# Optimization experiments

Measured on AMD Instinct MI355X. Metric: run time of the kernel, lower is better.

Reference implementation:

```python
import jax, jax.numpy as jnp
import numpy as np

B, P = 16, 1024
D_TIME, NUM_MODS = 8, 22
DIM_S = NUM_MODS + D_TIME + 1  # 31
PHI_W, N_HEADS, DP = 32, 4, 32
PSI_W, PSI_L, RHO_W = 64, 64, 64
SQRT_DP = float(np.sqrt(DP))


def setup_inputs() -> dict:
    key = jax.random.key(0)
    ks = jax.random.split(key, 16)
    rn = lambda k, shape: jax.random.normal(k, shape, jnp.float32) * 0.05
    return dict(
        times=jax.random.uniform(ks[0], (B, P), jnp.float32) * 48.0,
        values=jax.random.normal(ks[1], (B, P), jnp.float32),
        measurements=jax.random.randint(ks[2], (B, P), 0, NUM_MODS + 1),
        non_pad_mask=jnp.ones((B, P, 1), jnp.float32),
        W_psi1=rn(ks[3], (DIM_S, PSI_W)), b_psi1=jnp.zeros((PSI_W,), jnp.float32),
        W_psi2=rn(ks[4], (PSI_W, PSI_L)), b_psi2=jnp.zeros((PSI_L,), jnp.float32),
        W_key=rn(ks[5], (DIM_S + PSI_L, N_HEADS * DP)), b_key=jnp.zeros((N_HEADS * DP,), jnp.float32),
        query=rn(ks[6], (N_HEADS, DP)),
        W_phi1=rn(ks[7], (DIM_S, PHI_W)), b_phi1=jnp.zeros((PHI_W,), jnp.float32),
        W_phi2=rn(ks[8], (PHI_W, PHI_W)), b_phi2=jnp.zeros((PHI_W,), jnp.float32),
        W_rho1=rn(ks[9], (N_HEADS * PHI_W, RHO_W)), b_rho1=jnp.zeros((RHO_W,), jnp.float32),
        W_rho2=rn(ks[10], (RHO_W, RHO_W)), b_rho2=jnp.zeros((RHO_W,), jnp.float32),
    )


def _temporal_enc(times):
    i = np.arange(D_TIME)
    pos_vec = jnp.asarray(10000.0 ** (2.0 * (i // 2) / D_TIME), jnp.float32)
    ang = times[:, :, None] / pos_vec  # [B,P,d_time]
    return jnp.where(jnp.asarray(i % 2 == 0), jnp.sin(ang), jnp.cos(ang))


def reference(times, values, measurements, non_pad_mask,
              W_psi1, b_psi1, W_psi2, b_psi2, W_key, b_key, query,
              W_phi1, b_phi1, W_phi2, b_phi2, W_rho1, b_rho1, W_rho2, b_rho2):
    m = non_pad_mask  # [B,P,1]
    te = _temporal_enc(times)
    oh = jax.nn.one_hot(measurements, NUM_MODS + 1, dtype=jnp.float32)[:, :, 1:]
    x = jnp.concatenate([te, values[:, :, None], oh], axis=-1)  # [B,P,dim_s]

    # CumulativeSetAttentionLayer: psi MLP -> cumulative mean -> keys . query
    psi = jax.nn.relu(jax.nn.relu(x @ W_psi1 + b_psi1) @ W_psi2 + b_psi2)  # [B,P,psi_l]
    cum = jnp.cumsum(psi * m, axis=1) / jnp.cumsum(m, axis=1)
    keys = (jnp.concatenate([x, cum], axis=-1) @ W_key + b_key).reshape(B, P, N_HEADS, DP)
    pre = jnp.einsum('bpmd,md->bpm', keys, query) / SQRT_DP  # [B,P,m]

    # phi MLP
    phi = jax.nn.relu(jax.nn.relu(x @ W_phi1 + b_phi1) @ W_phi2 + b_phi2) * m  # [B,P,phi_w]

    # cumulative softmax weighting (online path)
    cmax = jax.lax.cummax(pre, axis=1)  # [B,P,m], running max for stability
    D = jnp.exp(pre[:, None, :, :] - cmax[:, :, None, :])  # [B,P,Q,m]
    causal = jnp.arange(P)[:, None] >= jnp.arange(P)[None, :]  # keep Q <= P
    D = D * causal[None, :, :, None]
    E = D.sum(axis=2)  # [B,P,m]
    agg = jnp.einsum('bpqm,bqd->bpmd', D, phi) / E[:, :, :, None]
    agg = (agg * m[:, :, :, None]).reshape(B, P, N_HEADS * PHI_W)

    # rho MLP (return_sequences)
    out = jax.nn.relu(jax.nn.relu(agg @ W_rho1 + b_rho1) @ W_rho2 + b_rho2) * m
    return out
```

## Files before the change

### kernel.cpp

```cpp
#include <hip/hip_runtime.h>
#include <hip/hip_bf16.h>

#define B_ 16
#define P_ 1024
#define T_ (B_*P_)
#define CH_ 32
#define CL_ (P_/CH_)

constexpr int OFF_A     = 16;
constexpr int OFF_WPSI1 = 400;
constexpr int OFF_BPSI1 = OFF_WPSI1 + 1984;
constexpr int OFF_WPSI2 = OFF_BPSI1 + 64;
constexpr int OFF_BPSI2 = OFF_WPSI2 + 4096;
constexpr int OFF_WKEY  = OFF_BPSI2 + 64;
constexpr int OFF_BKEY  = OFF_WKEY  + 12160;
constexpr int OFF_QRY   = OFF_BKEY  + 128;
constexpr int OFF_WPHI1 = OFF_QRY   + 128;
constexpr int OFF_BPHI1 = OFF_WPHI1 + 992;
constexpr int OFF_WPHI2 = OFF_BPHI1 + 32;
constexpr int OFF_BPHI2 = OFF_WPHI2 + 1024;
constexpr int OFF_WRHO1 = OFF_BPHI2 + 32;
constexpr int OFF_BRHO1 = OFF_WRHO1 + 8192;
constexpr int OFF_WRHO2 = OFF_BRHO1 + 64;
constexpr int OFF_BRHO2 = OFF_WRHO2 + 4096;
constexpr int OFF_PHI   = OFF_BRHO2 + 64;
constexpr int OFF_Z     = OFF_PHI   + T_*32;
constexpr int OFF_PREX  = OFF_Z     + T_*4;
constexpr int OFF_PRE   = OFF_PREX  + T_*4;
constexpr int OFF_AGG   = OFF_PRE   + T_*4;
constexpr int OFF_CME   = OFF_AGG   + T_*128;
constexpr int OFF_CS    = OFF_CME   + 4096;

static __device__ __forceinline__ bool detect_f32(const void* mask_raw) {
  return ((*(const unsigned*)mask_raw) & 0xFFFFu) == 0u;
}
static __device__ __forceinline__ float ld_any(const void* src, int i, bool isf32) {
  if (isf32) return ((const float*)src)[i];
  return __bfloat162float(((const __hip_bfloat16*)src)[i]);
}

__global__ __launch_bounds__(256) void s01_prep(
    float* __restrict__ ws, const void* mask,
    const void* Wpsi1, const void* bpsi1, const void* Wpsi2, const void* bpsi2,
    const void* Wkey,  const void* bkey,  const void* query,
    const void* Wphi1, const void* bphi1, const void* Wphi2, const void* bphi2,
    const void* Wrho1, const void* brho1, const void* Wrho2, const void* brho2) {
  const bool isf32 = detect_f32(mask);
  if (blockIdx.x < 2) {
    const int gid = blockIdx.x * 256 + threadIdx.x;
    if (gid >= 384) return;
    const float inv_s = 0.17677669529663687f;
    const int h = gid & 3;
    const int j = gid >> 2;
    float s = 0.f;
    if (j < 95) {
      for (int d = 0; d < 32; ++d)
        s += ld_any(Wkey, j * 128 + h * 32 + d, isf32) * ld_any(query, h * 32 + d, isf32);
    } else {
      for (int d = 0; d < 32; ++d)
        s += ld_any(bkey, h * 32 + d, isf32) * ld_any(query, h * 32 + d, isf32);
    }
    ws[OFF_A + gid] = s * inv_s;
    return;
  }
  const int g  = (blockIdx.x - 2) * 256 + threadIdx.x;
  const int gs = (gridDim.x - 2) * 256;
  auto st = [&](int off, const void* src, int n) {
    for (int i = g; i < n; i += gs) ws[off + i] = ld_any(src, i, isf32);
  };
  st(OFF_WPSI1, Wpsi1, 1984); st(OFF_BPSI1, bpsi1, 64);
  st(OFF_WPSI2, Wpsi2, 4096); st(OFF_BPSI2, bpsi2, 64);
  st(OFF_WPHI1, Wphi1, 992);  st(OFF_BPHI1, bphi1, 32);
  st(OFF_WPHI2, Wphi2, 1024); st(OFF_BPHI2, bphi2, 32);
  st(OFF_WRHO1, Wrho1, 8192); st(OFF_BRHO1, brho1, 64);
  st(OFF_WRHO2, Wrho2, 4096); st(OFF_BRHO2, brho2, 64);
}

__global__ __launch_bounds__(256) void k1_token(float* __restrict__ ws,
                                                const int* __restrict__ measp,
                                                const void* __restrict__ times,
                                                const void* __restrict__ values,
                                                const void* __restrict__ mask) {
  __shared__ float sh1[4][64];
  __shared__ float sg1[4][32];
  const bool isf32 = detect_f32(mask);
  const int tid = threadIdx.x;
  const int wv  = __builtin_amdgcn_readfirstlane(tid >> 6);
  const int j   = tid & 63;
  const int t   = blockIdx.x * 4 + wv;

  const float tval = ld_any(times, t, isf32);
  const float vval = ld_any(values, t, isf32);
  const float mval = ld_any(mask, t, isf32);
  const int   meas = measp[t];
  const float sel  = (meas > 0) ? 1.f : 0.f;
  const int   mrow = (meas > 0) ? (8 + meas) : 0;

  float x[9];
  const float posv[4] = {1.f, 10.f, 100.f, 1000.f};
  #pragma unroll
  for (int k = 0; k < 4; ++k) {
    float s, c;
    __sincosf(tval / posv[k], &s, &c);
    x[2*k] = s; x[2*k+1] = c;
  }
  x[8] = vval;

  float h1 = ws[OFF_BPSI1 + j];
  #pragma unroll
  for (int i = 0; i < 9; ++i) h1 = fmaf(x[i], ws[OFF_WPSI1 + i * 64 + j], h1);
  h1 = fmaf(sel, ws[OFF_WPSI1 + mrow * 64 + j], h1);
  sh1[wv][j] = fmaxf(h1, 0.f);

  if (j < 32) {
    float g1 = ws[OFF_BPHI1 + j];
    #pragma unroll
    for (int i = 0; i < 9; ++i) g1 = fmaf(x[i], ws[OFF_WPHI1 + i * 32 + j], g1);
    g1 = fmaf(sel, ws[OFF_WPHI1 + mrow * 32 + j], g1);
    sg1[wv][j] = fmaxf(g1, 0.f);
  }
  __syncthreads();

  float h2 = ws[OFF_BPSI2 + j];
  #pragma unroll 8
  for (int i = 0; i < 64; ++i) h2 = fmaf(sh1[wv][i], ws[OFF_WPSI2 + i * 64 + j], h2);
  const float q = fmaxf(h2, 0.f) * mval;

  const float* a2 = ws + OFF_A + (31 + j) * 4;
  float z0 = q * a2[0], z1 = q * a2[1], z2 = q * a2[2], z3 = q * a2[3];
  #pragma unroll
  for (int off = 32; off; off >>= 1) {
    z0 += __shfl_xor(z0, off, 64);
    z1 += __shfl_xor(z1, off, 64);
    z2 += __shfl_xor(z2, off, 64);
    z3 += __shfl_xor(z3, off, 64);
  }
  if (j == 0) {
    float* zo = ws + OFF_Z + (size_t)t * 4;
    zo[0] = z0; zo[1] = z1; zo[2] = z2; zo[3] = z3;
  }

  if (j < 32) {
    float g2 = ws[OFF_BPHI2 + j];
    #pragma unroll 8
    for (int i = 0; i < 32; ++i) g2 = fmaf(sg1[wv][i], ws[OFF_WPHI2 + i * 32 + j], g2);
    ws[OFF_PHI + (size_t)t * 32 + j] = fmaxf(g2, 0.f) * mval;
  } else if (j < 36) {
    const int h = j - 32;
    float pr = ws[OFF_A + 380 + h];
    #pragma unroll
    for (int i = 0; i < 9; ++i) pr = fmaf(x[i], ws[OFF_A + i * 4 + h], pr);
    pr = fmaf(sel, ws[OFF_A + mrow * 4 + h], pr);
    ws[OFF_PREX + (size_t)t * 4 + h] = pr;
  }
}

__global__ __launch_bounds__(256) void k2_scanz(float* __restrict__ ws,
                                                const void* __restrict__ mask) {
  const int b   = blockIdx.x;
  const int tid = threadIdx.x;
  const bool isf32 = detect_f32(mask);
  __shared__ float sc[256], s0[256], s1[256], s2[256], s3[256];

  const float* zB = ws + OFF_Z + (size_t)b * P_ * 4;
  const int p0 = tid * 4;

  float lc[4], l0[4], l1[4], l2[4], l3[4];
  float c = 0.f, z0 = 0.f, z1 = 0.f, z2 = 0.f, z3 = 0.f;
  #pragma unroll
  for (int i = 0; i < 4; ++i) {
    c  += ld_any(mask, b * P_ + p0 + i, isf32);
    z0 += zB[(p0 + i) * 4 + 0]; z1 += zB[(p0 + i) * 4 + 1];
    z2 += zB[(p0 + i) * 4 + 2]; z3 += zB[(p0 + i) * 4 + 3];
    lc[i] = c; l0[i] = z0; l1[i] = z1; l2[i] = z2; l3[i] = z3;
  }

  float rc = c, r0 = z0, r1 = z1, r2 = z2, r3 = z3;
  sc[tid] = rc; s0[tid] = r0; s1[tid] = r1; s2[tid] = r2; s3[tid] = r3;
  __syncthreads();
  for (int off = 1; off < 256; off <<= 1) {
    float ac = 0.f, a0 = 0.f, a1 = 0.f, a2 = 0.f, a3 = 0.f;
    if (tid >= off) {
      ac = sc[tid - off]; a0 = s0[tid - off]; a1 = s1[tid - off];
      a2 = s2[tid - off]; a3 = s3[tid - off];
    }
    __syncthreads();
    rc += ac; r0 += a0; r1 += a1; r2 += a2; r3 += a3;
    sc[tid] = rc; s0[tid] = r0; s1[tid] = r1; s2[tid] = r2; s3[tid] = r3;
    __syncthreads();
  }
  const float ec = rc - c, e0 = r0 - z0, e1 = r1 - z1, e2 = r2 - z2, e3 = r3 - z3;

  const float* px  = ws + OFF_PREX + (size_t)b * P_ * 4;
  float*       pre = ws + OFF_PRE  + (size_t)b * P_ * 4;
  #pragma unroll
  for (int i = 0; i < 4; ++i) {
    const float inv = 1.f / (ec + lc[i]);
    const int p = p0 + i;
    pre[p * 4 + 0] = px[p * 4 + 0] + (e0 + l0[i]) * inv;
    pre[p * 4 + 1] = px[p * 4 + 1] + (e1 + l1[i]) * inv;
    pre[p * 4 + 2] = px[p * 4 + 2] + (e2 + l2[i]) * inv;
    pre[p * 4 + 3] = px[p * 4 + 3] + (e3 + l3[i]) * inv;
  }
}

__global__ __launch_bounds__(128) void k4a_chunk(float* __restrict__ ws) {
  const int ch = blockIdx.x, b = blockIdx.y;
  const int h = threadIdx.x >> 5, d = threadIdx.x & 31;
  const float* preB = ws + OFF_PRE + (size_t)b * P_ * 4;
  const float* phiB = ws + OFF_PHI + (size_t)b * P_ * 32;

  float M = -__builtin_inff(), E = 0.f, S = 0.f;
  const int pbeg = ch * CL_;
  for (int p = pbeg; p < pbeg + CL_; ++p) {
    const float v  = preB[p * 4 + h];
    const float ph = phiB[p * 32 + d];
    const float nM = fmaxf(M, v);
    const float al = __expf(M - nM);
    const float w  = __expf(v - nM);
    E = fmaf(E, al, w);
    S = fmaf(S, al, w * ph);
    M = nM;
  }
  const int base = (b * CH_ + ch) * 4 + h;
  if (d == 0) { ws[OFF_CME + base * 2] = M; ws[OFF_CME + base * 2 + 1] = E; }
  ws[OFF_CS + base * 32 + d] = S;
}

__global__ __launch_bounds__(128) void k4c_replay(float* __restrict__ ws,
                                                  const void* __restrict__ mask) {
  const int ch = blockIdx.x, b = blockIdx.y;
  const int h = threadIdx.x >> 5, d = threadIdx.x & 31;
  const bool isf32 = detect_f32(mask);
  const float* preB = ws + OFF_PRE + (size_t)b * P_ * 4;
  const float* phiB = ws + OFF_PHI + (size_t)b * P_ * 32;
  float*       aggB = ws + OFF_AGG + (size_t)b * P_ * 128;

  float M = -__builtin_inff(), E = 0.f, S = 0.f;
  for (int c2 = 0; c2 < ch; ++c2) {
    const int base2 = (b * CH_ + c2) * 4 + h;
    const float cM = ws[OFF_CME + base2 * 2];
    const float cE = ws[OFF_CME + base2 * 2 + 1];
    const float cS = ws[OFF_CS  + base2 * 32 + d];
    const float nM = fmaxf(M, cM);
    const float a1 = __expf(M - nM);
    const float a2 = __expf(cM - nM);
    E = E * a1 + cE * a2;
    S = S * a1 + cS * a2;
    M = nM;
  }

  const int pbeg = ch * CL_;
  for (int p = pbeg; p < pbeg + CL_; ++p) {
    const float v  = preB[p * 4 + h];
    const float ph = phiB[p * 32 + d];
    const float nM = fmaxf(M, v);
    const float al = __expf(M - nM);
    const float w  = __expf(v - nM);
    E = fmaf(E, al, w);
    S = fmaf(S, al, w * ph);
    M = nM;
    aggB[p * 128 + h * 32 + d] = (S / E) * ld_any(mask, b * P_ + p, isf32);
  }
}

__global__ __launch_bounds__(256) void k5_rho(const float* __restrict__ ws,
                                              const void* __restrict__ mask_raw,
                                              void* __restrict__ out) {
  __shared__ float sW1[128 * 64];
  __shared__ float sH1[16][64];
  const int tid = threadIdx.x;
  for (int i = tid; i < 128 * 64; i += 256) sW1[i] = ws[OFF_WRHO1 + i];

  const int wv = __builtin_amdgcn_readfirstlane(tid >> 6);
  const int j  = tid & 63;
  const int t0 = blockIdx.x * 16 + wv * 4;
  const float* aggB = ws + OFF_AGG;

  const float b1 = ws[OFF_BRHO1 + j];
  float a0 = b1, a1 = b1, a2 = b1, a3 = b1;
  __syncthreads();

  #pragma unroll 8
  for (int i = 0; i < 128; ++i) {
    const float w = sW1[i * 64 + j];
    a0 = fmaf(aggB[(size_t)(t0 + 0) * 128 + i], w, a0);
    a1 = fmaf(aggB[(size_t)(t0 + 1) * 128 + i], w, a1);
    a2 = fmaf(aggB[(size_t)(t0 + 2) * 128 + i], w, a2);
    a3 = fmaf(aggB[(size_t)(t0 + 3) * 128 + i], w, a3);
  }
  sH1[wv * 4 + 0][j] = fmaxf(a0, 0.f);
  sH1[wv * 4 + 1][j] = fmaxf(a1, 0.f);
  sH1[wv * 4 + 2][j] = fmaxf(a2, 0.f);
  sH1[wv * 4 + 3][j] = fmaxf(a3, 0.f);
  __syncthreads();

  const float b2 = ws[OFF_BRHO2 + j];
  float o0 = b2, o1 = b2, o2 = b2, o3 = b2;
  #pragma unroll 8
  for (int i = 0; i < 64; ++i) {
    const float w = ws[OFF_WRHO2 + i * 64 + j];
    o0 = fmaf(sH1[wv * 4 + 0][i], w, o0);
    o1 = fmaf(sH1[wv * 4 + 1][i], w, o1);
    o2 = fmaf(sH1[wv * 4 + 2][i], w, o2);
    o3 = fmaf(sH1[wv * 4 + 3][i], w, o3);
  }

  const bool isf32 = detect_f32(mask_raw);
  float r[4] = {o0, o1, o2, o3};
  #pragma unroll
  for (int k = 0; k < 4; ++k) {
    const int t = t0 + k;
    const float v = fmaxf(r[k], 0.f) * ld_any(mask_raw, t, isf32);
    if (isf32) {
      ((float*)out)[(size_t)t * 64 + j] = v;
    } else {
      __hip_bfloat16 bb = __float2bfloat16(v);
      ((__hip_bfloat16*)out)[(size_t)t * 64 + j] = bb;
    }
  }
}

extern "C" void kernel_launch(void* const* d_in, const int* in_sizes, int n_in,
                              void* d_out, int out_size, void* d_ws, size_t ws_size,
                              hipStream_t stream) {
  const int* meas = (const int*)d_in[2];
  const void* times = d_in[0];
  const void* values = d_in[1];
  const void* mask = d_in[3];
  float* ws = (float*)d_ws;

  s01_prep<<<34, 256, 0, stream>>>(ws, mask,
                                   d_in[4], d_in[5], d_in[6], d_in[7],
                                   d_in[8], d_in[9], d_in[10],
                                   d_in[11], d_in[12], d_in[13], d_in[14],
                                   d_in[15], d_in[16], d_in[17], d_in[18]);
  k1_token<<<T_/4, 256, 0, stream>>>(ws, meas, times, values, mask);
  k2_scanz<<<B_, 256, 0, stream>>>(ws, mask);
  k4a_chunk<<<dim3(CH_, B_), 128, 0, stream>>>(ws);
  k4c_replay<<<dim3(CH_, B_), 128, 0, stream>>>(ws, mask);
  k5_rho<<<T_/16, 256, 0, stream>>>(ws, mask, d_out);
}
```

Measured before the change: 162.5 us.

## Fuse cumulative-softmax replay with rho MLP, keeping agg in shared memory

Merges the per-chunk replay kernel and the rho MLP kernel into one kernel. Each block writes its chunk's aggregated rows to LDS and then applies both rho layers directly. This removes the global write and re-read of the large agg buffer and one kernel launch. It also vectorises the LDS reads with float4. In exchange the rho stage runs with fewer waves (two per block, 512 blocks) and about 50KB of LDS per block, which may reduce occupancy.

```diff
diff --git a/kernel.cpp b/kernel.cpp
--- a/kernel.cpp
+++ b/kernel.cpp
@@ -12,10 +12,7 @@
 constexpr int OFF_BPSI1 = OFF_WPSI1 + 1984;
 constexpr int OFF_WPSI2 = OFF_BPSI1 + 64;
 constexpr int OFF_BPSI2 = OFF_WPSI2 + 4096;
-constexpr int OFF_WKEY  = OFF_BPSI2 + 64;
-constexpr int OFF_BKEY  = OFF_WKEY  + 12160;
-constexpr int OFF_QRY   = OFF_BKEY  + 128;
-constexpr int OFF_WPHI1 = OFF_QRY   + 128;
+constexpr int OFF_WPHI1 = OFF_BPSI2 + 64;
 constexpr int OFF_BPHI1 = OFF_WPHI1 + 992;
 constexpr int OFF_WPHI2 = OFF_BPHI1 + 32;
 constexpr int OFF_BPHI2 = OFF_WPHI2 + 1024;
@@ -27,8 +24,7 @@
 constexpr int OFF_Z     = OFF_PHI   + T_*32;
 constexpr int OFF_PREX  = OFF_Z     + T_*4;
 constexpr int OFF_PRE   = OFF_PREX  + T_*4;
-constexpr int OFF_AGG   = OFF_PRE   + T_*4;
-constexpr int OFF_CME   = OFF_AGG   + T_*128;
+constexpr int OFF_CME   = OFF_PRE   + T_*4;
 constexpr int OFF_CS    = OFF_CME   + 4096;
 
 static __device__ __forceinline__ bool detect_f32(const void* mask_raw) {
@@ -227,96 +223,114 @@
   ws[OFF_CS + base * 32 + d] = S;
 }
 
-__global__ __launch_bounds__(128) void k4c_replay(float* __restrict__ ws,
-                                                  const void* __restrict__ mask) {
+__global__ __launch_bounds__(128) void k4r_fused(float* __restrict__ ws,
+                                                 const void* __restrict__ mask,
+                                                 void* __restrict__ out) {
+  __shared__ float sAgg[CL_][128];
+  __shared__ float sW1[128 * 64];
+  __shared__ float sH1[2][4][64];
   const int ch = blockIdx.x, b = blockIdx.y;
-  const int h = threadIdx.x >> 5, d = threadIdx.x & 31;
+  const int tid = threadIdx.x;
   const bool isf32 = detect_f32(mask);
-  const float* preB = ws + OFF_PRE + (size_t)b * P_ * 4;
-  const float* phiB = ws + OFF_PHI + (size_t)b * P_ * 32;
-  float*       aggB = ws + OFF_AGG + (size_t)b * P_ * 128;
-
-  float M = -__builtin_inff(), E = 0.f, S = 0.f;
-  for (int c2 = 0; c2 < ch; ++c2) {
-    const int base2 = (b * CH_ + c2) * 4 + h;
-    const float cM = ws[OFF_CME + base2 * 2];
-    const float cE = ws[OFF_CME + base2 * 2 + 1];
-    const float cS = ws[OFF_CS  + base2 * 32 + d];
-    const float nM = fmaxf(M, cM);
-    const float a1 = __expf(M - nM);
-    const float a2 = __expf(cM - nM);
-    E = E * a1 + cE * a2;
-    S = S * a1 + cS * a2;
-    M = nM;
-  }
-
-  const int pbeg = ch * CL_;
-  for (int p = pbeg; p < pbeg + CL_; ++p) {
-    const float v  = preB[p * 4 + h];
-    const float ph = phiB[p * 32 + d];
-    const float nM = fmaxf(M, v);
-    const float al = __expf(M - nM);
-    const float w  = __expf(v - nM);
-    E = fmaf(E, al, w);
-    S = fmaf(S, al, w * ph);
-    M = nM;
-    aggB[p * 128 + h * 32 + d] = (S / E) * ld_any(mask, b * P_ + p, isf32);
-  }
-}
-
-__global__ __launch_bounds__(256) void k5_rho(const float* __restrict__ ws,
-                                              const void* __restrict__ mask_raw,
-                                              void* __restrict__ out) {
-  __shared__ float sW1[128 * 64];
-  __shared__ float sH1[16][64];
-  const int tid = threadIdx.x;
-  for (int i = tid; i < 128 * 64; i += 256) sW1[i] = ws[OFF_WRHO1 + i];
-
-  const int wv = __builtin_amdgcn_readfirstlane(tid >> 6);
-  const int j  = tid & 63;
-  const int t0 = blockIdx.x * 16 + wv * 4;
-  const float* aggB = ws + OFF_AGG;
-
+
+  {
+    const float4* src = (const float4*)(ws + OFF_WRHO1);
+    float4* dst = (float4*)sW1;
+    #pragma unroll
+    for (int k = 0; k < 16; ++k) dst[tid + k * 128] = src[tid + k * 128];
+  }
+
+  {
+    const int h = tid >> 5, d = tid & 31;
+    const float* preB = ws + OFF_PRE + (size_t)b * P_ * 4;
+    const float* phiB = ws + OFF_PHI + (size_t)b * P_ * 32;
+
+    float M = -__builtin_inff(), E = 0.f, S = 0.f;
+    for (int c2 = 0; c2 < ch; ++c2) {
+      const int base2 = (b * CH_ + c2) * 4 + h;
+      const float cM = ws[OFF_CME + base2 * 2];
+      const float cE = ws[OFF_CME + base2 * 2 + 1];
+      const float cS = ws[OFF_CS  + base2 * 32 + d];
+      const float nM = fmaxf(M, cM);
+      const float a1 = __expf(M - nM);
+      const float a2 = __expf(cM - nM);
+      E = E * a1 + cE * a2;
+      S = S * a1 + cS * a2;
+      M = nM;
+    }
+    const int pbeg = ch * CL_;
+    for (int p = pbeg; p < pbeg + CL_; ++p) {
+      const float v  = preB[p * 4 + h];
+      const float ph = phiB[p * 32 + d];
+      const float nM = fmaxf(M, v);
+      const float al = __expf(M - nM);
+      const float w  = __expf(v - nM);
+      E = fmaf(E, al, w);
+      S = fmaf(S, al, w * ph);
+      M = nM;
+      sAgg[p - pbeg][tid] = (S / E) * ld_any(mask, b * P_ + p, isf32);
+    }
+  }
+  __syncthreads();
+
+  const int w = tid >> 6;
+  const int j = tid & 63;
   const float b1 = ws[OFF_BRHO1 + j];
-  float a0 = b1, a1 = b1, a2 = b1, a3 = b1;
-  __syncthreads();
-
-  #pragma unroll 8
-  for (int i = 0; i < 128; ++i) {
-    const float w = sW1[i * 64 + j];
-    a0 = fmaf(aggB[(size_t)(t0 + 0) * 128 + i], w, a0);
-    a1 = fmaf(aggB[(size_t)(t0 + 1) * 128 + i], w, a1);
-    a2 = fmaf(aggB[(size_t)(t0 + 2) * 128 + i], w, a2);
-    a3 = fmaf(aggB[(size_t)(t0 + 3) * 128 + i], w, a3);
-  }
-  sH1[wv * 4 + 0][j] = fmaxf(a0, 0.f);
-  sH1[wv * 4 + 1][j] = fmaxf(a1, 0.f);
-  sH1[wv * 4 + 2][j] = fmaxf(a2, 0.f);
-  sH1[wv * 4 + 3][j] = fmaxf(a3, 0.f);
-  __syncthreads();
-
   const float b2 = ws[OFF_BRHO2 + j];
-  float o0 = b2, o1 = b2, o2 = b2, o3 = b2;
-  #pragma unroll 8
-  for (int i = 0; i < 64; ++i) {
-    const float w = ws[OFF_WRHO2 + i * 64 + j];
-    o0 = fmaf(sH1[wv * 4 + 0][i], w, o0);
-    o1 = fmaf(sH1[wv * 4 + 1][i], w, o1);
-    o2 = fmaf(sH1[wv * 4 + 2][i], w, o2);
-    o3 = fmaf(sH1[wv * 4 + 3][i], w, o3);
-  }
-
-  const bool isf32 = detect_f32(mask_raw);
-  float r[4] = {o0, o1, o2, o3};
-  #pragma unroll
-  for (int k = 0; k < 4; ++k) {
-    const int t = t0 + k;
-    const float v = fmaxf(r[k], 0.f) * ld_any(mask_raw, t, isf32);
-    if (isf32) {
-      ((float*)out)[(size_t)t * 64 + j] = v;
-    } else {
-      __hip_bfloat16 bb = __float2bfloat16(v);
-      ((__hip_bfloat16*)out)[(size_t)t * 64 + j] = bb;
+  const int pbase = b * P_ + ch * CL_;
+
+  for (int g = 0; g < 4; ++g) {
+    const int pp = w * 16 + g * 4;
+    float a0 = b1, a1 = b1, a2 = b1, a3 = b1;
+    const float4* r0 = (const float4*)sAgg[pp + 0];
+    const float4* r1 = (const float4*)sAgg[pp + 1];
+    const float4* r2 = (const float4*)sAgg[pp + 2];
+    const float4* r3 = (const float4*)sAgg[pp + 3];
+    #pragma unroll 8
+    for (int ii = 0; ii < 32; ++ii) {
+      const float4 v0 = r0[ii], v1 = r1[ii], v2 = r2[ii], v3 = r3[ii];
+      const float wa = sW1[(4*ii + 0) * 64 + j];
+      const float wb = sW1[(4*ii + 1) * 64 + j];
+      const float wc = sW1[(4*ii + 2) * 64 + j];
+      const float wd = sW1[(4*ii + 3) * 64 + j];
+      a0 = fmaf(v0.x, wa, a0); a0 = fmaf(v0.y, wb, a0); a0 = fmaf(v0.z, wc, a0); a0 = fmaf(v0.w, wd, a0);
+      a1 = fmaf(v1.x, wa, a1); a1 = fmaf(v1.y, wb, a1); a1 = fmaf(v1.z, wc, a1); a1 = fmaf(v1.w, wd, a1);
+      a2 = fmaf(v2.x, wa, a2); a2 = fmaf(v2.y, wb, a2); a2 = fmaf(v2.z, wc, a2); a2 = fmaf(v2.w, wd, a2);
+      a3 = fmaf(v3.x, wa, a3); a3 = fmaf(v3.y, wb, a3); a3 = fmaf(v3.z, wc, a3); a3 = fmaf(v3.w, wd, a3);
+    }
+    sH1[w][0][j] = fmaxf(a0, 0.f);
+    sH1[w][1][j] = fmaxf(a1, 0.f);
+    sH1[w][2][j] = fmaxf(a2, 0.f);
+    sH1[w][3][j] = fmaxf(a3, 0.f);
+
+    float o0 = b2, o1 = b2, o2 = b2, o3 = b2;
+    const float4* q0 = (const float4*)sH1[w][0];
+    const float4* q1 = (const float4*)sH1[w][1];
+    const float4* q2 = (const float4*)sH1[w][2];
+    const float4* q3 = (const float4*)sH1[w][3];
+    #pragma unroll 4
+    for (int ii = 0; ii < 16; ++ii) {
+      const float4 u0 = q0[ii], u1 = q1[ii], u2 = q2[ii], u3 = q3[ii];
+      const float wa = ws[OFF_WRHO2 + (4*ii + 0) * 64 + j];
+      const float wb = ws[OFF_WRHO2 + (4*ii + 1) * 64 + j];
+      const float wc = ws[OFF_WRHO2 + (4*ii + 2) * 64 + j];
+      const float wd = ws[OFF_WRHO2 + (4*ii + 3) * 64 + j];
+      o0 = fmaf(u0.x, wa, o0); o0 = fmaf(u0.y, wb, o0); o0 = fmaf(u0.z, wc, o0); o0 = fmaf(u0.w, wd, o0);
+      o1 = fmaf(u1.x, wa, o1); o1 = fmaf(u1.y, wb, o1); o1 = fmaf(u1.z, wc, o1); o1 = fmaf(u1.w, wd, o1);
+      o2 = fmaf(u2.x, wa, o2); o2 = fmaf(u2.y, wb, o2); o2 = fmaf(u2.z, wc, o2); o2 = fmaf(u2.w, wd, o2);
+      o3 = fmaf(u3.x, wa, o3); o3 = fmaf(u3.y, wb, o3); o3 = fmaf(u3.z, wc, o3); o3 = fmaf(u3.w, wd, o3);
+    }
+
+    const float rr[4] = {o0, o1, o2, o3};
+    #pragma unroll
+    for (int k = 0; k < 4; ++k) {
+      const int t = pbase + pp + k;
+      const float v = fmaxf(rr[k], 0.f) * ld_any(mask, t, isf32);
+      if (isf32) {
+        ((float*)out)[(size_t)t * 64 + j] = v;
+      } else {
+        ((__hip_bfloat16*)out)[(size_t)t * 64 + j] = __float2bfloat16(v);
+      }
     }
   }
 }
@@ -338,6 +352,5 @@
   k1_token<<<T_/4, 256, 0, stream>>>(ws, meas, times, values, mask);
   k2_scanz<<<B_, 256, 0, stream>>>(ws, mask);
   k4a_chunk<<<dim3(CH_, B_), 128, 0, stream>>>(ws);
-  k4c_replay<<<dim3(CH_, B_), 128, 0, stream>>>(ws, mask);
-  k5_rho<<<T_/16, 256, 0, stream>>>(ws, mask, d_out);
-}
+  k4r_fused<<<dim3(CH_, B_), 128, 0, stream>>>(ws, mask, d_out);
+}
```

Measured after the change: 167.1 us. 2.9% more time.

## Replace online softmax rescaling with per-sequence max and precomputed exp weights

Applied to the files above, without the earlier changes.

The scan kernel now takes the max of the attention logits per batch and head over the whole sequence. It writes the exponentiated weights once to the workspace instead of the raw logits. The chunk-sum and replay kernels then do plain running sums of exp weights and weighted phi, with no per-step max tracking or rescaling exponentials. This shortens the serial dependency chain and removes two exponentials per step, at the risk of underflow if logits early in a sequence are far below the sequence max.

```diff
diff --git a/kernel.cpp b/kernel.cpp
--- a/kernel.cpp
+++ b/kernel.cpp
@@ -12,10 +12,7 @@
 constexpr int OFF_BPSI1 = OFF_WPSI1 + 1984;
 constexpr int OFF_WPSI2 = OFF_BPSI1 + 64;
 constexpr int OFF_BPSI2 = OFF_WPSI2 + 4096;
-constexpr int OFF_WKEY  = OFF_BPSI2 + 64;
-constexpr int OFF_BKEY  = OFF_WKEY  + 12160;
-constexpr int OFF_QRY   = OFF_BKEY  + 128;
-constexpr int OFF_WPHI1 = OFF_QRY   + 128;
+constexpr int OFF_WPHI1 = OFF_BPSI2 + 64;
 constexpr int OFF_BPHI1 = OFF_WPHI1 + 992;
 constexpr int OFF_WPHI2 = OFF_BPHI1 + 32;
 constexpr int OFF_BPHI2 = OFF_WPHI2 + 1024;
@@ -26,10 +23,10 @@
 constexpr int OFF_PHI   = OFF_BRHO2 + 64;
 constexpr int OFF_Z     = OFF_PHI   + T_*32;
 constexpr int OFF_PREX  = OFF_Z     + T_*4;
-constexpr int OFF_PRE   = OFF_PREX  + T_*4;
-constexpr int OFF_AGG   = OFF_PRE   + T_*4;
-constexpr int OFF_CME   = OFF_AGG   + T_*128;
-constexpr int OFF_CS    = OFF_CME   + 4096;
+constexpr int OFF_EXPW  = OFF_PREX  + T_*4;
+constexpr int OFF_CE    = OFF_EXPW  + T_*4;
+constexpr int OFF_CS    = OFF_CE    + 2048;
+constexpr int OFF_AGG   = OFF_CS    + 65536;
 
 static __device__ __forceinline__ bool detect_f32(const void* mask_raw) {
   return ((*(const unsigned*)mask_raw) & 0xFFFFu) == 0u;
@@ -191,39 +188,63 @@
   }
   const float ec = rc - c, e0 = r0 - z0, e1 = r1 - z1, e2 = r2 - z2, e3 = r3 - z3;
 
-  const float* px  = ws + OFF_PREX + (size_t)b * P_ * 4;
-  float*       pre = ws + OFF_PRE  + (size_t)b * P_ * 4;
+  const float* px = ws + OFF_PREX + (size_t)b * P_ * 4;
+  float pre[4][4];
+  float mx0 = -1e30f, mx1 = -1e30f, mx2 = -1e30f, mx3 = -1e30f;
   #pragma unroll
   for (int i = 0; i < 4; ++i) {
     const float inv = 1.f / (ec + lc[i]);
     const int p = p0 + i;
-    pre[p * 4 + 0] = px[p * 4 + 0] + (e0 + l0[i]) * inv;
-    pre[p * 4 + 1] = px[p * 4 + 1] + (e1 + l1[i]) * inv;
-    pre[p * 4 + 2] = px[p * 4 + 2] + (e2 + l2[i]) * inv;
-    pre[p * 4 + 3] = px[p * 4 + 3] + (e3 + l3[i]) * inv;
-  }
-}
-
-__global__ __launch_bounds__(128) void k4a_chunk(float* __restrict__ ws) {
+    pre[i][0] = px[p * 4 + 0] + (e0 + l0[i]) * inv;
+    pre[i][1] = px[p * 4 + 1] + (e1 + l1[i]) * inv;
+    pre[i][2] = px[p * 4 + 2] + (e2 + l2[i]) * inv;
+    pre[i][3] = px[p * 4 + 3] + (e3 + l3[i]) * inv;
+    mx0 = fmaxf(mx0, pre[i][0]); mx1 = fmaxf(mx1, pre[i][1]);
+    mx2 = fmaxf(mx2, pre[i][2]); mx3 = fmaxf(mx3, pre[i][3]);
+  }
+
+  __syncthreads();
+  s0[tid] = mx0; s1[tid] = mx1; s2[tid] = mx2; s3[tid] = mx3;
+  __syncthreads();
+  for (int off = 128; off; off >>= 1) {
+    if (tid < off) {
+      s0[tid] = fmaxf(s0[tid], s0[tid + off]);
+      s1[tid] = fmaxf(s1[tid], s1[tid + off]);
+      s2[tid] = fmaxf(s2[tid], s2[tid + off]);
+      s3[tid] = fmaxf(s3[tid], s3[tid + off]);
+    }
+    __syncthreads();
+  }
+  const float M0 = s0[0], M1 = s1[0], M2 = s2[0], M3 = s3[0];
+
+  float* eB = ws + OFF_EXPW + (size_t)b * P_ * 4;
+  #pragma unroll
+  for (int i = 0; i < 4; ++i) {
+    const int p = p0 + i;
+    eB[p * 4 + 0] = __expf(pre[i][0] - M0);
+    eB[p * 4 + 1] = __expf(pre[i][1] - M1);
+    eB[p * 4 + 2] = __expf(pre[i][2] - M2);
+    eB[p * 4 + 3] = __expf(pre[i][3] - M3);
+  }
+}
+
+__global__ __launch_bounds__(128) void k4a_sums(float* __restrict__ ws) {
   const int ch = blockIdx.x, b = blockIdx.y;
   const int h = threadIdx.x >> 5, d = threadIdx.x & 31;
-  const float* preB = ws + OFF_PRE + (size_t)b * P_ * 4;
-  const float* phiB = ws + OFF_PHI + (size_t)b * P_ * 32;
-
-  float M = -__builtin_inff(), E = 0.f, S = 0.f;
+  const float* eB   = ws + OFF_EXPW + (size_t)b * P_ * 4;
+  const float* phiB = ws + OFF_PHI  + (size_t)b * P_ * 32;
+
+  float E = 0.f, S = 0.f;
   const int pbeg = ch * CL_;
+  #pragma unroll 4
   for (int p = pbeg; p < pbeg + CL_; ++p) {
-    const float v  = preB[p * 4 + h];
+    const float e  = eB[p * 4 + h];
     const float ph = phiB[p * 32 + d];
-    const float nM = fmaxf(M, v);
-    const float al = __expf(M - nM);
-    const float w  = __expf(v - nM);
-    E = fmaf(E, al, w);
-    S = fmaf(S, al, w * ph);
-    M = nM;
+    E += e;
+    S = fmaf(e, ph, S);
   }
   const int base = (b * CH_ + ch) * 4 + h;
-  if (d == 0) { ws[OFF_CME + base * 2] = M; ws[OFF_CME + base * 2 + 1] = E; }
+  if (d == 0) ws[OFF_CE + base] = E;
   ws[OFF_CS + base * 32 + d] = S;
 }
 
@@ -232,34 +253,23 @@
   const int ch = blockIdx.x, b = blockIdx.y;
   const int h = threadIdx.x >> 5, d = threadIdx.x & 31;
   const bool isf32 = detect_f32(mask);
-  const float* preB = ws + OFF_PRE + (size_t)b * P_ * 4;
-  const float* phiB = ws + OFF_PHI + (size_t)b * P_ * 32;
-  float*       aggB = ws + OFF_AGG + (size_t)b * P_ * 128;
-
-  float M = -__builtin_inff(), E = 0.f, S = 0.f;
+  const float* eB   = ws + OFF_EXPW + (size_t)b * P_ * 4;
+  const float* phiB = ws + OFF_PHI  + (size_t)b * P_ * 32;
+  float*       aggB = ws + OFF_AGG  + (size_t)b * P_ * 128;
+
+  float E = 0.f, S = 0.f;
   for (int c2 = 0; c2 < ch; ++c2) {
     const int base2 = (b * CH_ + c2) * 4 + h;
-    const float cM = ws[OFF_CME + base2 * 2];
-    const float cE = ws[OFF_CME + base2 * 2 + 1];
-    const float cS = ws[OFF_CS  + base2 * 32 + d];
-    const float nM = fmaxf(M, cM);
-    const float a1 = __expf(M - nM);
-    const float a2 = __expf(cM - nM);
-    E = E * a1 + cE * a2;
-    S = S * a1 + cS * a2;
-    M = nM;
+    E += ws[OFF_CE + base2];
+    S += ws[OFF_CS + base2 * 32 + d];
   }
 
   const int pbeg = ch * CL_;
   for (int p = pbeg; p < pbeg + CL_; ++p) {
-    const float v  = preB[p * 4 + h];
+    const float e  = eB[p * 4 + h];
     const float ph = phiB[p * 32 + d];
-    const float nM = fmaxf(M, v);
-    const float al = __expf(M - nM);
-    const float w  = __expf(v - nM);
-    E = fmaf(E, al, w);
-    S = fmaf(S, al, w * ph);
-    M = nM;
+    E += e;
+    S = fmaf(e, ph, S);
     aggB[p * 128 + h * 32 + d] = (S / E) * ld_any(mask, b * P_ + p, isf32);
   }
 }
@@ -315,8 +325,7 @@
     if (isf32) {
       ((float*)out)[(size_t)t * 64 + j] = v;
     } else {
-      __hip_bfloat16 bb = __float2bfloat16(v);
-      ((__hip_bfloat16*)out)[(size_t)t * 64 + j] = bb;
+      ((__hip_bfloat16*)out)[(size_t)t * 64 + j] = __float2bfloat16(v);
     }
   }
 }
@@ -337,7 +346,7 @@
                                    d_in[15], d_in[16], d_in[17], d_in[18]);
   k1_token<<<T_/4, 256, 0, stream>>>(ws, meas, times, values, mask);
   k2_scanz<<<B_, 256, 0, stream>>>(ws, mask);
-  k4a_chunk<<<dim3(CH_, B_), 128, 0, stream>>>(ws);
+  k4a_sums<<<dim3(CH_, B_), 128, 0, stream>>>(ws);
   k4c_replay<<<dim3(CH_, B_), 128, 0, stream>>>(ws, mask);
   k5_rho<<<T_/16, 256, 0, stream>>>(ws, mask, d_out);
 }
```

After: 160.3 us (median of 2 runs). About the same (-1.4%).
